# Performance work log

Measured on AMD Instinct MI355X. Metric: run time of the kernel, lower is better.

Reference implementation:

```python
import jax, jax.numpy as jnp
import numpy as np

N, E, F_IN, F_HID, K = 100000, 1600000, 64, 64, 6


def setup_inputs() -> dict:
    key = jax.random.key(0)
    k1, k2, k3, k4, k5 = jax.random.split(key, 5)
    x = jax.random.normal(k1, (N, F_IN), dtype=jnp.float32)
    # edges with no self-loops (PyG ChebConv removes self loops before normalization)
    src = jax.random.randint(k2, (E,), 0, N, dtype=jnp.int32)
    off = jax.random.randint(k3, (E,), 1, N, dtype=jnp.int32)
    dst = (src + off) % N
    edge_index = jnp.stack([src, dst], axis=0)
    # Glorot-ish init for the K Chebyshev weight matrices
    W = jax.random.normal(k4, (K, F_IN, F_HID), dtype=jnp.float32) * (1.0 / np.sqrt(F_IN))
    b = jax.random.normal(k5, (F_HID,), dtype=jnp.float32) * 0.01
    return {"x": x, "edge_index": edge_index, "W": W, "b": b}


def reference(x, edge_index, W, b):
    # ChebConv with sym normalization, lambda_max = 2.0 (PyG default):
    # scaled Laplacian L_hat = 2*L/lambda_max - I = -D^{-1/2} A D^{-1/2} (zero diagonal)
    row = edge_index[0].astype(jnp.int32)  # source j
    col = edge_index[1].astype(jnp.int32)  # target i
    n = x.shape[0]
    deg = jax.ops.segment_sum(jnp.ones_like(row, dtype=x.dtype), row, num_segments=n)
    dinv = jnp.where(deg > 0, jax.lax.rsqrt(deg), jnp.zeros_like(deg))
    w = -(dinv[row] * dinv[col])  # [E] edge weights of L_hat

    def prop(h):  # h: [N, F] -> L_hat @ h via gather-scale-scatter
        return jax.ops.segment_sum(w[:, None] * h[row], col, num_segments=n)

    # Chebyshev recurrence: Tx_0 = x, Tx_1 = L_hat x, Tx_k = 2 L_hat Tx_{k-1} - Tx_{k-2}
    Tx0 = x
    out = Tx0 @ W[0]
    Tx1 = prop(Tx0)
    out = out + Tx1 @ W[1]
    for k in range(2, W.shape[0]):
        Tx2 = 2.0 * prop(Tx1) - Tx0
        out = out + Tx2 @ W[k]
        Tx0, Tx1 = Tx1, Tx2
    return jax.nn.relu(out + b)
```

## Files before the change

### kernel.cpp

```cpp
#include <hip/hip_runtime.h>


constexpr int F = 64;
constexpr int SCAN_ELEMS = 1024;
constexpr int BSH = 9;
constexpr int EPB = 2048;
constexpr int PNPW = 8;

typedef __attribute__((ext_vector_type(8))) short short8;
typedef __attribute__((ext_vector_type(4))) float floatx4;
typedef __attribute__((ext_vector_type(2))) float floatx2;

#if defined(__has_builtin)
#if __has_builtin(__builtin_amdgcn_cvt_pk_f32_fp8) && __has_builtin(__builtin_amdgcn_cvt_pk_fp8_f32)
#define HAVE_FP8 1
#endif
#endif
#ifndef HAVE_FP8
#define HAVE_FP8 0
#endif

__device__ __forceinline__ unsigned short f_to_bf(float f) {
    unsigned u = __float_as_uint(f);
    u += 0x7FFFu + ((u >> 16) & 1u);
    return (unsigned short)(u >> 16);
}
__device__ __forceinline__ float bf_to_f(unsigned short s) {
    return __uint_as_float(((unsigned)s) << 16);
}
__device__ __forceinline__ float4 bf4_to_f4(ushort4 u) {
    float4 f;
    f.x = bf_to_f(u.x); f.y = bf_to_f(u.y); f.z = bf_to_f(u.z); f.w = bf_to_f(u.w);
    return f;
}

#if HAVE_FP8
__device__ __forceinline__ float4 fp8x4_to_f4(unsigned u) {
    floatx2 lo = __builtin_amdgcn_cvt_pk_f32_fp8((int)u, false);
    floatx2 hi = __builtin_amdgcn_cvt_pk_f32_fp8((int)u, true);
    float4 f;
    f.x = lo.x; f.y = lo.y; f.z = hi.x; f.w = hi.y;
    return f;
}
__device__ __forceinline__ unsigned f4_to_fp8x4(float a, float b, float c, float d) {
    int pk = 0;
    pk = __builtin_amdgcn_cvt_pk_fp8_f32(a, b, pk, false);
    pk = __builtin_amdgcn_cvt_pk_fp8_f32(c, d, pk, true);
    return (unsigned)pk;
}
#else
__device__ __forceinline__ float4 fp8x4_to_f4(unsigned u) { return make_float4(0, 0, 0, 0); }
__device__ __forceinline__ unsigned f4_to_fp8x4(float a, float b, float c, float d) { return 0; }
#endif

__global__ void hist2_kernel(const int* __restrict__ row, const int* __restrict__ col,
                             int* __restrict__ gcH, int* __restrict__ gcS,
                             int P, int G, int E) {
    __shared__ int hH[256], hS[256];
    const int tid = threadIdx.x, blk = blockIdx.x;
    hH[tid] = 0; hS[tid] = 0;
    __syncthreads();
    const int start = blk * EPB + tid * 8;
    if (start + 7 < E) {
        const int4 c0 = *(const int4*)(col + start);
        const int4 c1 = *(const int4*)(col + start + 4);
        const int4 r0 = *(const int4*)(row + start);
        const int4 r1 = *(const int4*)(row + start + 4);
        atomicAdd(&hH[c0.x >> BSH], 1); atomicAdd(&hH[c0.y >> BSH], 1);
        atomicAdd(&hH[c0.z >> BSH], 1); atomicAdd(&hH[c0.w >> BSH], 1);
        atomicAdd(&hH[c1.x >> BSH], 1); atomicAdd(&hH[c1.y >> BSH], 1);
        atomicAdd(&hH[c1.z >> BSH], 1); atomicAdd(&hH[c1.w >> BSH], 1);
        atomicAdd(&hS[r0.x >> BSH], 1); atomicAdd(&hS[r0.y >> BSH], 1);
        atomicAdd(&hS[r0.z >> BSH], 1); atomicAdd(&hS[r0.w >> BSH], 1);
        atomicAdd(&hS[r1.x >> BSH], 1); atomicAdd(&hS[r1.y >> BSH], 1);
        atomicAdd(&hS[r1.z >> BSH], 1); atomicAdd(&hS[r1.w >> BSH], 1);
    } else {
        for (int k = start; k < E && k < start + 8; ++k) {
            atomicAdd(&hH[col[k] >> BSH], 1);
            atomicAdd(&hS[row[k] >> BSH], 1);
        }
    }
    __syncthreads();
    if (tid < P) {
        gcH[(size_t)tid * G + blk] = hH[tid];
        gcS[(size_t)tid * G + blk] = hS[tid];
    }
}

__device__ __forceinline__ int4 load_cnt4(const int* __restrict__ cnt, int i, int N) {
    int4 v = make_int4(0, 0, 0, 0);
    if (i + 3 < N) {
        v = *(const int4*)(cnt + i);
    } else {
        if (i + 0 < N) v.x = cnt[i + 0];
        if (i + 1 < N) v.y = cnt[i + 1];
        if (i + 2 < N) v.z = cnt[i + 2];
        if (i + 3 < N) v.w = cnt[i + 3];
    }
    return v;
}

__global__ void scan1_kernel(const int* __restrict__ cnt, int* __restrict__ bsum, int N) {
    const int tid = threadIdx.x;
    const int i = blockIdx.x * SCAN_ELEMS + tid * 4;
    int4 v = load_cnt4(cnt, i, N);
    int s = v.x + v.y + v.z + v.w;
#pragma unroll
    for (int off = 1; off < 64; off <<= 1) s += __shfl_xor(s, off);
    __shared__ int ws[4];
    if ((tid & 63) == 0) ws[tid >> 6] = s;
    __syncthreads();
    if (tid == 0) bsum[blockIdx.x] = ws[0] + ws[1] + ws[2] + ws[3];
}

__global__ void scan2_kernel(const int* __restrict__ bsum, int* __restrict__ boff,
                             int* __restrict__ total_out, int nb) {
    const int tid = threadIdx.x;
    const int lane = tid & 63, w = tid >> 6;
    int v = (tid < nb) ? bsum[tid] : 0;
    int inc = v;
#pragma unroll
    for (int off = 1; off < 64; off <<= 1) {
        int t = __shfl_up(inc, off);
        if (lane >= off) inc += t;
    }
    __shared__ int wsum[4];
    if (lane == 63) wsum[w] = inc;
    __syncthreads();
    int wo = 0;
    for (int k = 0; k < w; ++k) wo += wsum[k];
    const int excl = wo + inc - v;
    if (tid < nb) boff[tid] = excl;
    if (tid == nb - 1) *total_out = excl + v;
}

__global__ void scan3_kernel(const int* __restrict__ cnt, const int* __restrict__ boff,
                             int* __restrict__ dst, int N) {
    const int tid = threadIdx.x;
    const int lane = tid & 63, w = tid >> 6;
    const int i = blockIdx.x * SCAN_ELEMS + tid * 4;
    int4 v = load_cnt4(cnt, i, N);
    const int s = v.x + v.y + v.z + v.w;
    int inc = s;
#pragma unroll
    for (int off = 1; off < 64; off <<= 1) {
        int t = __shfl_up(inc, off);
        if (lane >= off) inc += t;
    }
    __shared__ int wsum[4];
    if (lane == 63) wsum[w] = inc;
    __syncthreads();
    int wo = 0;
    for (int k = 0; k < w; ++k) wo += wsum[k];
    const int r0 = boff[blockIdx.x] + wo + inc - s;
    const int r1 = r0 + v.x, r2 = r1 + v.y, r3 = r2 + v.z;
    if (i + 3 < N) {
        *(int4*)(dst + i) = make_int4(r0, r1, r2, r3);
    } else {
        if (i + 0 < N) dst[i + 0] = r0;
        if (i + 1 < N) dst[i + 1] = r1;
        if (i + 2 < N) dst[i + 2] = r2;
        if (i + 3 < N) dst[i + 3] = r3;
    }
}

__global__ void part2_kernel(const int* __restrict__ row, const int* __restrict__ col,
                             const int* __restrict__ goH, const int* __restrict__ goS,
                             int* __restrict__ partH, int* __restrict__ partS,
                             int P, int G, int E) {
    __shared__ int cH[256], cS[256];
    const int tid = threadIdx.x, blk = blockIdx.x;
    if (tid < P) {
        cH[tid] = goH[(size_t)tid * G + blk];
        cS[tid] = goS[(size_t)tid * G + blk];
    }
    __syncthreads();
    const int start = blk * EPB + tid * 8;
    for (int k = start; k < E && k < start + 8; ++k) {
        const int c = col[k], r = row[k];
        const int posH = atomicAdd(&cH[c >> BSH], 1);
        partH[posH] = ((c & ((1 << BSH) - 1)) << 23) | r;
        const int posS = atomicAdd(&cS[r >> BSH], 1);
        partS[posS] = r;
    }
}

__global__ void bucketC_kernel(const int* __restrict__ part, const int* __restrict__ goff,
                               int* __restrict__ rowptr, int* __restrict__ csr,
                               int P, int G, int N, int E) {
    __shared__ int cnt[512];
    __shared__ int excl[512];
    __shared__ int wsum[4];
    const int tid = threadIdx.x;
    const int b = blockIdx.x;
    const int base_node = b << BSH;
    const int nn = min(512, N - base_node);
    const int estart = goff[(size_t)b * G];
    const int eend = (b + 1 < P) ? goff[(size_t)(b + 1) * G] : E;

    cnt[tid] = 0; cnt[tid + 256] = 0;
    __syncthreads();
    for (int i = estart + tid; i < eend; i += 256)
        atomicAdd(&cnt[((unsigned)part[i]) >> 23], 1);
    __syncthreads();
    {
        const int lane = tid & 63, w = tid >> 6;
        const int a0 = cnt[2 * tid], a1 = cnt[2 * tid + 1];
        const int ps = a0 + a1;
        int inc = ps;
#pragma unroll
        for (int off = 1; off < 64; off <<= 1) {
            int t = __shfl_up(inc, off);
            if (lane >= off) inc += t;
        }
        if (lane == 63) wsum[w] = inc;
        __syncthreads();
        int wo = 0;
        for (int k = 0; k < w; ++k) wo += wsum[k];
        const int ep = wo + inc - ps;
        excl[2 * tid] = ep;
        excl[2 * tid + 1] = ep + a0;
    }
    __syncthreads();
    if (tid < nn) rowptr[base_node + tid] = estart + excl[tid];
    for (int ln = 256 + tid; ln < nn; ln += 256) rowptr[base_node + ln] = estart + excl[ln];
    if (b == P - 1 && tid == 0) rowptr[N] = E;
    cnt[tid] = 0; cnt[tid + 256] = 0;
    __syncthreads();
    for (int i = estart + tid; i < eend; i += 256) {
        const int pk = part[i];
        const int ln = ((unsigned)pk) >> 23;
        const int pos = atomicAdd(&cnt[ln], 1);
        csr[estart + excl[ln] + pos] = pk & 0x7FFFFF;
    }
}

__global__ void bucketD_kernel(const int* __restrict__ partS, const int* __restrict__ goffS,
                               float* __restrict__ dinv, float* __restrict__ dinv2,
                               float* __restrict__ rdinv, int P, int G, int N, int E) {
    __shared__ int cnt[512];
    const int tid = threadIdx.x;
    const int b = blockIdx.x;
    const int base_node = b << BSH;
    const int nn = min(512, N - base_node);
    const int estart = goffS[(size_t)b * G];
    const int eend = (b + 1 < P) ? goffS[(size_t)(b + 1) * G] : E;
    cnt[tid] = 0; cnt[tid + 256] = 0;
    __syncthreads();
    for (int i = estart + tid; i < eend; i += 256)
        atomicAdd(&cnt[partS[i] - base_node], 1);
    __syncthreads();
    for (int l = tid; l < nn; l += 256) {
        const int dI = cnt[l];
        const float d = (float)dI;
        const bool ok = dI > 0;
        dinv[base_node + l]  = ok ? rsqrtf(d) : 0.0f;
        dinv2[base_node + l] = ok ? 1.0f / d : 0.0f;
        rdinv[base_node + l] = ok ? sqrtf(d) : 0.0f;
    }
}

__global__ void init_s0_kernel(const float* __restrict__ dinv, const float* __restrict__ x,
                               unsigned short* __restrict__ S0b, unsigned char* __restrict__ S0f8,
                               int NF, int write8) {
    int i = blockIdx.x * blockDim.x + threadIdx.x;
    int j = i * 4;
    if (j >= NF) return;
    const float dv = dinv[j >> 6];
    const float4 v = *(const float4*)(x + j);
    const float a = dv * v.x, bb = dv * v.y, c = dv * v.z, d = dv * v.w;
    ushort4 u;
    u.x = f_to_bf(a); u.y = f_to_bf(bb); u.z = f_to_bf(c); u.w = f_to_bf(d);
    *(ushort4*)(S0b + j) = u;
    if (write8) *(unsigned*)(S0f8 + j) = f4_to_fp8x4(a, bb, c, d);
}

template <int FIRST>
__global__ __launch_bounds__(256, 6)
void prop_g4(const int* __restrict__ rowptr, const int* __restrict__ csr,
             const float* __restrict__ dinv2, const unsigned short* __restrict__ Sprev,
             const unsigned short* __restrict__ Sm2, unsigned short* __restrict__ Sk, int N) {
    const int lane = threadIdx.x & 63;
    const int g16 = lane & 48;
    const int fl = lane & 15;
    const int wave = threadIdx.x >> 6;
    const int wbase = (blockIdx.x * 4 + wave) * PNPW;
    for (int j = 0; j < PNPW; j += 4) {
        const int n = wbase + j + (g16 >> 4);
        const bool nv = n < N;
        const int nc = nv ? n : N - 1;
        const int s = rowptr[nc], e = rowptr[nc + 1];
        const int len = e - s;
        float4 acc = {0.f, 0.f, 0.f, 0.f};
        for (int c = 0; c < len; c += 16) {
            const int ii = s + c + fl;
            const int idxv = csr[ii < e ? ii : e - 1];
            const int mm = min(16, len - c);
            ushort4 u[16];
#pragma unroll
            for (int t = 0; t < 16; ++t) {
                const int it = __shfl(idxv, g16 + t);
                u[t] = *(const ushort4*)(Sprev + (size_t)it * F + fl * 4);
            }
#pragma unroll
            for (int t = 0; t < 16; ++t) {
                if (t < mm) {
                    const float4 v = bf4_to_f4(u[t]);
                    acc.x += v.x; acc.y += v.y; acc.z += v.z; acc.w += v.w;
                }
            }
        }
        if (nv) {
            const float d2 = dinv2[n];
            float4 sn;
            if (FIRST) {
                sn.x = -d2 * acc.x; sn.y = -d2 * acc.y;
                sn.z = -d2 * acc.z; sn.w = -d2 * acc.w;
            } else {
                const float4 m2 = bf4_to_f4(*(const ushort4*)(Sm2 + (size_t)n * F + fl * 4));
                sn.x = -2.f * d2 * acc.x - m2.x; sn.y = -2.f * d2 * acc.y - m2.y;
                sn.z = -2.f * d2 * acc.z - m2.z; sn.w = -2.f * d2 * acc.w - m2.w;
            }
            ushort4 o;
            o.x = f_to_bf(sn.x); o.y = f_to_bf(sn.y);
            o.z = f_to_bf(sn.z); o.w = f_to_bf(sn.w);
            *(ushort4*)(Sk + (size_t)n * F + fl * 4) = o;
        }
    }
}

template <int FIRST, int W8>
__global__ __launch_bounds__(256, 6)
void prop_f8(const int* __restrict__ rowptr, const int* __restrict__ csr,
             const float* __restrict__ dinv2, const unsigned char* __restrict__ S8prev,
             const unsigned short* __restrict__ Sm2, unsigned short* __restrict__ Sk,
             unsigned char* __restrict__ Sk8, int N) {
    const int lane = threadIdx.x & 63;
    const int g16 = lane & 48;
    const int fl = lane & 15;
    const int wave = threadIdx.x >> 6;
    const int wbase = (blockIdx.x * 4 + wave) * PNPW;
    for (int j = 0; j < PNPW; j += 4) {
        const int n = wbase + j + (g16 >> 4);
        const bool nv = n < N;
        const int nc = nv ? n : N - 1;
        const int s = rowptr[nc], e = rowptr[nc + 1];
        const int len = e - s;
        float4 acc = {0.f, 0.f, 0.f, 0.f};
        for (int c = 0; c < len; c += 16) {
            const int ii = s + c + fl;
            const int idxv = csr[ii < e ? ii : e - 1];
            const int mm = min(16, len - c);
            unsigned u[16];
#pragma unroll
            for (int t = 0; t < 16; ++t) {
                const int it = __shfl(idxv, g16 + t);
                u[t] = *(const unsigned*)(S8prev + (size_t)it * F + fl * 4);
            }
#pragma unroll
            for (int t = 0; t < 16; ++t) {
                if (t < mm) {
                    const float4 v = fp8x4_to_f4(u[t]);
                    acc.x += v.x; acc.y += v.y; acc.z += v.z; acc.w += v.w;
                }
            }
        }
        if (nv) {
            const float d2 = dinv2[n];
            float4 sn;
            if (FIRST) {
                sn.x = -d2 * acc.x; sn.y = -d2 * acc.y;
                sn.z = -d2 * acc.z; sn.w = -d2 * acc.w;
            } else {
                const float4 m2 = bf4_to_f4(*(const ushort4*)(Sm2 + (size_t)n * F + fl * 4));
                sn.x = -2.f * d2 * acc.x - m2.x; sn.y = -2.f * d2 * acc.y - m2.y;
                sn.z = -2.f * d2 * acc.z - m2.z; sn.w = -2.f * d2 * acc.w - m2.w;
            }
            ushort4 o;
            o.x = f_to_bf(sn.x); o.y = f_to_bf(sn.y);
            o.z = f_to_bf(sn.z); o.w = f_to_bf(sn.w);
            *(ushort4*)(Sk + (size_t)n * F + fl * 4) = o;
            if (W8) *(unsigned*)(Sk8 + (size_t)n * F + fl * 4) = f4_to_fp8x4(sn.x, sn.y, sn.z, sn.w);
        }
    }
}

__global__ void wfrag_kernel(const float* __restrict__ W, unsigned short* __restrict__ Wfrag) {
    const int idx = blockIdx.x * blockDim.x + threadIdx.x;
    if (idx >= 4 * 12 * 64) return;
    const int lane = idx & 63;
    const int s = (idx >> 6) % 12;
    const int ft = idx / (64 * 12);
    const int n = ft * 16 + (lane & 15);
    const int quad = lane >> 4;
    unsigned short v[8];
#pragma unroll
    for (int j = 0; j < 8; ++j) {
        const int kg = s * 32 + quad * 8 + j;
        const int kk = kg >> 6, f = kg & 63;
        v[j] = f_to_bf(W[kk * F * F + f * F + n]);
    }
    ushort4 lo = {v[0], v[1], v[2], v[3]};
    ushort4 hi = {v[4], v[5], v[6], v[7]};
    *(ushort4*)(Wfrag + (size_t)idx * 8) = lo;
    *(ushort4*)(Wfrag + (size_t)idx * 8 + 4) = hi;
}

__global__ __launch_bounds__(256, 3)
void mfma_out_kernel(const float* __restrict__ x, const unsigned short* __restrict__ Sstack,
                     const unsigned short* __restrict__ Wfrag, const float* __restrict__ rdinv,
                     const float* __restrict__ dinv2, const float* __restrict__ W,
                     const float* __restrict__ b, float* __restrict__ out, int N, int NF) {
    const int lane = threadIdx.x & 63;
    const int wave = threadIdx.x >> 6;
    const int quad = lane >> 4;
    const int fl = lane & 15;
    const int tm = (blockIdx.x * 4 + wave) * 16;
    if (tm >= N) return;
    const int ma = tm + fl;
    const int mac = ma < N ? ma : N - 1;

    const unsigned short* sa = Sstack + (size_t)mac * F + quad * 8;

    short8 Afr[12];
#pragma unroll
    for (int s = 0; s < 12; ++s) {
        const int kk = s >> 1, f0 = (s & 1) * 32;
        Afr[s] = *(const short8*)(sa + (size_t)kk * NF + f0);
    }

    floatx4 C0 = {0.f, 0.f, 0.f, 0.f};
    floatx4 C1 = {0.f, 0.f, 0.f, 0.f};
    floatx4 C2 = {0.f, 0.f, 0.f, 0.f};
    floatx4 C3 = {0.f, 0.f, 0.f, 0.f};
    const unsigned short* wf = Wfrag + (size_t)lane * 8;
#pragma unroll
    for (int s = 0; s < 12; ++s) {
        const short8 B0 = *(const short8*)(wf + (size_t)(0 * 12 + s) * 64 * 8);
        const short8 B1 = *(const short8*)(wf + (size_t)(1 * 12 + s) * 64 * 8);
        const short8 B2 = *(const short8*)(wf + (size_t)(2 * 12 + s) * 64 * 8);
        const short8 B3 = *(const short8*)(wf + (size_t)(3 * 12 + s) * 64 * 8);
        C0 = __builtin_amdgcn_mfma_f32_16x16x32_bf16(Afr[s], B0, C0, 0, 0, 0);
        C1 = __builtin_amdgcn_mfma_f32_16x16x32_bf16(Afr[s], B1, C1, 0, 0, 0);
        C2 = __builtin_amdgcn_mfma_f32_16x16x32_bf16(Afr[s], B2, C2, 0, 0, 0);
        C3 = __builtin_amdgcn_mfma_f32_16x16x32_bf16(Afr[s], B3, C3, 0, 0, 0);
    }

    const float bl0 = b[0 * 16 + fl];
    const float bl1 = b[1 * 16 + fl];
    const float bl2 = b[2 * 16 + fl];
    const float bl3 = b[3 * 16 + fl];

#pragma unroll
    for (int r = 0; r < 4; ++r) {
        const int m = tm + quad * 4 + r;
        if (m >= N) continue;
        const float rs = rdinv[m];
        const bool z = (dinv2[m] == 0.0f);
        float v0 = rs * C0[r], v1 = rs * C1[r], v2 = rs * C2[r], v3 = rs * C3[r];
        if (z) {
            const float* xr = x + (size_t)m * F;
            float f0 = 0.f, f1 = 0.f, f2 = 0.f, f3 = 0.f;
            for (int f = 0; f < F; ++f) {
                const float xv = xr[f];
                const float* w0 = W + 0 * F * F + f * F;
                const float* w2 = W + 2 * F * F + f * F;
                const float* w4 = W + 4 * F * F + f * F;
                f0 += xv * (w0[0 * 16 + fl] - w2[0 * 16 + fl] + w4[0 * 16 + fl]);
                f1 += xv * (w0[1 * 16 + fl] - w2[1 * 16 + fl] + w4[1 * 16 + fl]);
                f2 += xv * (w0[2 * 16 + fl] - w2[2 * 16 + fl] + w4[2 * 16 + fl]);
                f3 += xv * (w0[3 * 16 + fl] - w2[3 * 16 + fl] + w4[3 * 16 + fl]);
            }
            v0 = f0; v1 = f1; v2 = f2; v3 = f3;
        }
        float* orow = out + (size_t)m * F;
        orow[0 * 16 + fl] = fmaxf(v0 + bl0, 0.f);
        orow[1 * 16 + fl] = fmaxf(v1 + bl1, 0.f);
        orow[2 * 16 + fl] = fmaxf(v2 + bl2, 0.f);
        orow[3 * 16 + fl] = fmaxf(v3 + bl3, 0.f);
    }
}

extern "C" void kernel_launch(void* const* d_in, const int* in_sizes, int n_in,
                              void* d_out, int out_size, void* d_ws, size_t ws_size,
                              hipStream_t stream) {
    const float* x = (const float*)d_in[0];
    const int* ei = (const int*)d_in[1];
    const float* W = (const float*)d_in[2];
    const float* b = (const float*)d_in[3];

    const int N = in_sizes[0] / F;
    const int E = in_sizes[1] / 2;
    const int NF = N * F;
    const int* row = ei;
    const int* col = ei + E;

    const int P = (N + 511) >> BSH;
    const int G = (E + EPB - 1) / EPB;
    const int M = P * G;

    char* p = (char*)d_ws;
    auto alloc = [&](size_t bytes) {
        char* r = p;
        p += (bytes + 63) & ~(size_t)63;
        return r;
    };
    float* dinv   = (float*)alloc((size_t)N * sizeof(float));
    float* dinv2  = (float*)alloc((size_t)N * sizeof(float));
    float* rdinv  = (float*)alloc((size_t)N * sizeof(float));
    int*   rowptr = (int*)alloc((size_t)(N + 1) * sizeof(int));
    int*   bsum   = (int*)alloc(256 * sizeof(int));
    int*   boff   = (int*)alloc(256 * sizeof(int));
    int*   totS   = (int*)alloc(64);
    int*   gcH    = (int*)alloc((size_t)M * sizeof(int));
    int*   goH    = (int*)alloc((size_t)M * sizeof(int));
    int*   gcS    = (int*)alloc((size_t)M * sizeof(int));
    int*   goS    = (int*)alloc((size_t)M * sizeof(int));
    int*   csr    = (int*)alloc((size_t)E * sizeof(int));
    unsigned short* Sstack = (unsigned short*)alloc((size_t)6 * NF * sizeof(unsigned short));
    unsigned short* Wfrag  = (unsigned short*)alloc((size_t)4 * 12 * 64 * 8 * sizeof(unsigned short));
    unsigned char* F8A = (unsigned char*)alloc((size_t)NF);
    unsigned char* F8B = (unsigned char*)alloc((size_t)NF);
    const size_t needed = (size_t)(p - (char*)d_ws);
    const bool pathA = HAVE_FP8 && ws_size >= needed;
    int* partH = (int*)Sstack;
    int* partS = (int*)(Sstack + (size_t)NF);
    float* out = (float*)d_out;

    const int B = 256;
    const int nsbM = (M + SCAN_ELEMS - 1) / SCAN_ELEMS;
    const int pgrid = (N + 4 * PNPW - 1) / (4 * PNPW);

    hist2_kernel<<<G, B, 0, stream>>>(row, col, gcH, gcS, P, G, E);
    scan1_kernel<<<nsbM, B, 0, stream>>>(gcH, bsum, M);
    scan2_kernel<<<1, B, 0, stream>>>(bsum, boff, rowptr + N, nsbM);
    scan3_kernel<<<nsbM, B, 0, stream>>>(gcH, boff, goH, M);
    scan1_kernel<<<nsbM, B, 0, stream>>>(gcS, bsum, M);
    scan2_kernel<<<1, B, 0, stream>>>(bsum, boff, totS, nsbM);
    scan3_kernel<<<nsbM, B, 0, stream>>>(gcS, boff, goS, M);
    part2_kernel<<<G, B, 0, stream>>>(row, col, goH, goS, partH, partS, P, G, E);
    bucketC_kernel<<<P, B, 0, stream>>>(partH, goH, rowptr, csr, P, G, N, E);
    bucketD_kernel<<<P, B, 0, stream>>>(partS, goS, dinv, dinv2, rdinv, P, G, N, E);

    wfrag_kernel<<<(4 * 12 * 64 + B - 1) / B, B, 0, stream>>>(W, Wfrag);
    init_s0_kernel<<<(NF / 4 + B - 1) / B, B, 0, stream>>>(dinv, x, Sstack, F8A, NF,
                                                           pathA ? 1 : 0);
    unsigned short* S1 = Sstack + (size_t)1 * NF;
    unsigned short* S2 = Sstack + (size_t)2 * NF;
    unsigned short* S3 = Sstack + (size_t)3 * NF;
    unsigned short* S4 = Sstack + (size_t)4 * NF;
    unsigned short* S5 = Sstack + (size_t)5 * NF;
    if (pathA) {
        prop_f8<1, 1><<<pgrid, B, 0, stream>>>(rowptr, csr, dinv2, F8A, Sstack, S1, F8B, N);
        prop_f8<0, 1><<<pgrid, B, 0, stream>>>(rowptr, csr, dinv2, F8B, Sstack, S2, F8A, N);
        prop_f8<0, 1><<<pgrid, B, 0, stream>>>(rowptr, csr, dinv2, F8A, S1, S3, F8B, N);
        prop_f8<0, 1><<<pgrid, B, 0, stream>>>(rowptr, csr, dinv2, F8B, S2, S4, F8A, N);
        prop_f8<0, 0><<<pgrid, B, 0, stream>>>(rowptr, csr, dinv2, F8A, S3, S5, F8B, N);
    } else {
        prop_g4<1><<<pgrid, B, 0, stream>>>(rowptr, csr, dinv2, Sstack, Sstack, S1, N);
        prop_g4<0><<<pgrid, B, 0, stream>>>(rowptr, csr, dinv2, S1, Sstack, S2, N);
        prop_g4<0><<<pgrid, B, 0, stream>>>(rowptr, csr, dinv2, S2, S1, S3, N);
        prop_g4<0><<<pgrid, B, 0, stream>>>(rowptr, csr, dinv2, S3, S2, S4, N);
        prop_g4<0><<<pgrid, B, 0, stream>>>(rowptr, csr, dinv2, S4, S3, S5, N);
    }
    mfma_out_kernel<<<(N + 63) / 64, 256, 0, stream>>>(x, Sstack, Wfrag, rdinv, dinv2,
                                                       W, b, out, N, NF);
}
```

Measured before the change: 368.0 us.

## Split propagation into two source-node halves for cache locality

Each CSR row is split by source index into a low half (below N/2) and a high half, with a new midptr array marking the boundary. Every propagation step becomes two kernels: one gathers from low-index sources and writes fp32 partial sums to a buffer, the other gathers from high-index sources, adds the partials and finishes the Chebyshev update. The aim is to keep each pass's gather working set (half the feature table) resident in cache. In exchange it doubles kernel launches, adds an fp32 N×64 partial buffer write and read per step, and halves per-row work, which can leave lanes underused on short rows.

```diff
diff --git a/kernel.cpp b/kernel.cpp
--- a/kernel.cpp
+++ b/kernel.cpp
@@ -186,9 +186,12 @@
 }
 
 __global__ void bucketC_kernel(const int* __restrict__ part, const int* __restrict__ goff,
-                               int* __restrict__ rowptr, int* __restrict__ csr,
-                               int P, int G, int N, int E) {
+                               int* __restrict__ rowptr, int* __restrict__ midptr,
+                               int* __restrict__ csr,
+                               int P, int G, int N, int E, int H) {
     __shared__ int cnt[512];
+    __shared__ int cntA[512];
+    __shared__ int cursB[512];
     __shared__ int excl[512];
     __shared__ int wsum[4];
     const int tid = threadIdx.x;
@@ -199,9 +202,15 @@
     const int eend = (b + 1 < P) ? goff[(size_t)(b + 1) * G] : E;
 
     cnt[tid] = 0; cnt[tid + 256] = 0;
-    __syncthreads();
-    for (int i = estart + tid; i < eend; i += 256)
-        atomicAdd(&cnt[((unsigned)part[i]) >> 23], 1);
+    cntA[tid] = 0; cntA[tid + 256] = 0;
+    cursB[tid] = 0; cursB[tid + 256] = 0;
+    __syncthreads();
+    for (int i = estart + tid; i < eend; i += 256) {
+        const int pk = part[i];
+        const int ln = ((unsigned)pk) >> 23;
+        atomicAdd(&cnt[ln], 1);
+        if ((pk & 0x7FFFFF) < H) atomicAdd(&cntA[ln], 1);
+    }
     __syncthreads();
     {
         const int lane = tid & 63, w = tid >> 6;
@@ -222,16 +231,24 @@
         excl[2 * tid + 1] = ep + a0;
     }
     __syncthreads();
-    if (tid < nn) rowptr[base_node + tid] = estart + excl[tid];
-    for (int ln = 256 + tid; ln < nn; ln += 256) rowptr[base_node + ln] = estart + excl[ln];
+    for (int ln = tid; ln < nn; ln += 256) {
+        rowptr[base_node + ln] = estart + excl[ln];
+        midptr[base_node + ln] = estart + excl[ln] + cntA[ln];
+    }
     if (b == P - 1 && tid == 0) rowptr[N] = E;
     cnt[tid] = 0; cnt[tid + 256] = 0;
     __syncthreads();
     for (int i = estart + tid; i < eend; i += 256) {
         const int pk = part[i];
         const int ln = ((unsigned)pk) >> 23;
-        const int pos = atomicAdd(&cnt[ln], 1);
-        csr[estart + excl[ln] + pos] = pk & 0x7FFFFF;
+        const int r = pk & 0x7FFFFF;
+        if (r < H) {
+            const int pos = atomicAdd(&cnt[ln], 1);
+            csr[estart + excl[ln] + pos] = r;
+        } else {
+            const int pos = atomicAdd(&cursB[ln], 1);
+            csr[estart + excl[ln] + cntA[ln] + pos] = r;
+        }
     }
 }
 
@@ -275,11 +292,11 @@
     if (write8) *(unsigned*)(S0f8 + j) = f4_to_fp8x4(a, bb, c, d);
 }
 
-template <int FIRST>
+
 __global__ __launch_bounds__(256, 6)
-void prop_g4(const int* __restrict__ rowptr, const int* __restrict__ csr,
-             const float* __restrict__ dinv2, const unsigned short* __restrict__ Sprev,
-             const unsigned short* __restrict__ Sm2, unsigned short* __restrict__ Sk, int N) {
+void propA_g4(const int* __restrict__ rowptr, const int* __restrict__ midp,
+              const int* __restrict__ csr, const unsigned short* __restrict__ Sprev,
+              float* __restrict__ accP, int N) {
     const int lane = threadIdx.x & 63;
     const int g16 = lane & 48;
     const int fl = lane & 15;
@@ -289,7 +306,7 @@
         const int n = wbase + j + (g16 >> 4);
         const bool nv = n < N;
         const int nc = nv ? n : N - 1;
-        const int s = rowptr[nc], e = rowptr[nc + 1];
+        const int s = rowptr[nc], e = midp[nc];
         const int len = e - s;
         float4 acc = {0.f, 0.f, 0.f, 0.f};
         for (int c = 0; c < len; c += 16) {
@@ -310,7 +327,49 @@
                 }
             }
         }
+        if (nv) *(float4*)(accP + (size_t)n * F + fl * 4) = acc;
+    }
+}
+
+template <int FIRST>
+__global__ __launch_bounds__(256, 6)
+void propB_g4(const int* __restrict__ rowptr, const int* __restrict__ midp,
+              const int* __restrict__ csr, const float* __restrict__ dinv2,
+              const unsigned short* __restrict__ Sprev, const float* __restrict__ accP,
+              const unsigned short* __restrict__ Sm2, unsigned short* __restrict__ Sk, int N) {
+    const int lane = threadIdx.x & 63;
+    const int g16 = lane & 48;
+    const int fl = lane & 15;
+    const int wave = threadIdx.x >> 6;
+    const int wbase = (blockIdx.x * 4 + wave) * PNPW;
+    for (int j = 0; j < PNPW; j += 4) {
+        const int n = wbase + j + (g16 >> 4);
+        const bool nv = n < N;
+        const int nc = nv ? n : N - 1;
+        const int s = midp[nc], e = rowptr[nc + 1];
+        const int len = e - s;
+        float4 acc = {0.f, 0.f, 0.f, 0.f};
+        for (int c = 0; c < len; c += 16) {
+            const int ii = s + c + fl;
+            const int idxv = csr[ii < e ? ii : e - 1];
+            const int mm = min(16, len - c);
+            ushort4 u[16];
+#pragma unroll
+            for (int t = 0; t < 16; ++t) {
+                const int it = __shfl(idxv, g16 + t);
+                u[t] = *(const ushort4*)(Sprev + (size_t)it * F + fl * 4);
+            }
+#pragma unroll
+            for (int t = 0; t < 16; ++t) {
+                if (t < mm) {
+                    const float4 v = bf4_to_f4(u[t]);
+                    acc.x += v.x; acc.y += v.y; acc.z += v.z; acc.w += v.w;
+                }
+            }
+        }
         if (nv) {
+            const float4 pa = *(const float4*)(accP + (size_t)n * F + fl * 4);
+            acc.x += pa.x; acc.y += pa.y; acc.z += pa.z; acc.w += pa.w;
             const float d2 = dinv2[n];
             float4 sn;
             if (FIRST) {
@@ -329,12 +388,10 @@
     }
 }
 
-template <int FIRST, int W8>
 __global__ __launch_bounds__(256, 6)
-void prop_f8(const int* __restrict__ rowptr, const int* __restrict__ csr,
-             const float* __restrict__ dinv2, const unsigned char* __restrict__ S8prev,
-             const unsigned short* __restrict__ Sm2, unsigned short* __restrict__ Sk,
-             unsigned char* __restrict__ Sk8, int N) {
+void propA_f8(const int* __restrict__ rowptr, const int* __restrict__ midp,
+              const int* __restrict__ csr, const unsigned char* __restrict__ S8prev,
+              float* __restrict__ accP, int N) {
     const int lane = threadIdx.x & 63;
     const int g16 = lane & 48;
     const int fl = lane & 15;
@@ -344,7 +401,7 @@
         const int n = wbase + j + (g16 >> 4);
         const bool nv = n < N;
         const int nc = nv ? n : N - 1;
-        const int s = rowptr[nc], e = rowptr[nc + 1];
+        const int s = rowptr[nc], e = midp[nc];
         const int len = e - s;
         float4 acc = {0.f, 0.f, 0.f, 0.f};
         for (int c = 0; c < len; c += 16) {
@@ -365,7 +422,50 @@
                 }
             }
         }
+        if (nv) *(float4*)(accP + (size_t)n * F + fl * 4) = acc;
+    }
+}
+
+template <int FIRST, int W8>
+__global__ __launch_bounds__(256, 6)
+void propB_f8(const int* __restrict__ rowptr, const int* __restrict__ midp,
+              const int* __restrict__ csr, const float* __restrict__ dinv2,
+              const unsigned char* __restrict__ S8prev, const float* __restrict__ accP,
+              const unsigned short* __restrict__ Sm2, unsigned short* __restrict__ Sk,
+              unsigned char* __restrict__ Sk8, int N) {
+    const int lane = threadIdx.x & 63;
+    const int g16 = lane & 48;
+    const int fl = lane & 15;
+    const int wave = threadIdx.x >> 6;
+    const int wbase = (blockIdx.x * 4 + wave) * PNPW;
+    for (int j = 0; j < PNPW; j += 4) {
+        const int n = wbase + j + (g16 >> 4);
+        const bool nv = n < N;
+        const int nc = nv ? n : N - 1;
+        const int s = midp[nc], e = rowptr[nc + 1];
+        const int len = e - s;
+        float4 acc = {0.f, 0.f, 0.f, 0.f};
+        for (int c = 0; c < len; c += 16) {
+            const int ii = s + c + fl;
+            const int idxv = csr[ii < e ? ii : e - 1];
+            const int mm = min(16, len - c);
+            unsigned u[16];
+#pragma unroll
+            for (int t = 0; t < 16; ++t) {
+                const int it = __shfl(idxv, g16 + t);
+                u[t] = *(const unsigned*)(S8prev + (size_t)it * F + fl * 4);
+            }
+#pragma unroll
+            for (int t = 0; t < 16; ++t) {
+                if (t < mm) {
+                    const float4 v = fp8x4_to_f4(u[t]);
+                    acc.x += v.x; acc.y += v.y; acc.z += v.z; acc.w += v.w;
+                }
+            }
+        }
         if (nv) {
+            const float4 pa = *(const float4*)(accP + (size_t)n * F + fl * 4);
+            acc.x += pa.x; acc.y += pa.y; acc.z += pa.z; acc.w += pa.w;
             const float d2 = dinv2[n];
             float4 sn;
             if (FIRST) {
@@ -498,6 +598,7 @@
     const int P = (N + 511) >> BSH;
     const int G = (E + EPB - 1) / EPB;
     const int M = P * G;
+    const int H = N >> 1;
 
     char* p = (char*)d_ws;
     auto alloc = [&](size_t bytes) {
@@ -509,6 +610,7 @@
     float* dinv2  = (float*)alloc((size_t)N * sizeof(float));
     float* rdinv  = (float*)alloc((size_t)N * sizeof(float));
     int*   rowptr = (int*)alloc((size_t)(N + 1) * sizeof(int));
+    int*   midptr = (int*)alloc((size_t)N * sizeof(int));
     int*   bsum   = (int*)alloc(256 * sizeof(int));
     int*   boff   = (int*)alloc(256 * sizeof(int));
     int*   totS   = (int*)alloc(64);
@@ -519,6 +621,7 @@
     int*   csr    = (int*)alloc((size_t)E * sizeof(int));
     unsigned short* Sstack = (unsigned short*)alloc((size_t)6 * NF * sizeof(unsigned short));
     unsigned short* Wfrag  = (unsigned short*)alloc((size_t)4 * 12 * 64 * 8 * sizeof(unsigned short));
+    float* accP = (float*)alloc((size_t)NF * sizeof(float));
     unsigned char* F8A = (unsigned char*)alloc((size_t)NF);
     unsigned char* F8B = (unsigned char*)alloc((size_t)NF);
     const size_t needed = (size_t)(p - (char*)d_ws);
@@ -539,7 +642,7 @@
     scan2_kernel<<<1, B, 0, stream>>>(bsum, boff, totS, nsbM);
     scan3_kernel<<<nsbM, B, 0, stream>>>(gcS, boff, goS, M);
     part2_kernel<<<G, B, 0, stream>>>(row, col, goH, goS, partH, partS, P, G, E);
-    bucketC_kernel<<<P, B, 0, stream>>>(partH, goH, rowptr, csr, P, G, N, E);
+    bucketC_kernel<<<P, B, 0, stream>>>(partH, goH, rowptr, midptr, csr, P, G, N, E, H);
     bucketD_kernel<<<P, B, 0, stream>>>(partS, goS, dinv, dinv2, rdinv, P, G, N, E);
 
     wfrag_kernel<<<(4 * 12 * 64 + B - 1) / B, B, 0, stream>>>(W, Wfrag);
@@ -551,17 +654,37 @@
     unsigned short* S4 = Sstack + (size_t)4 * NF;
     unsigned short* S5 = Sstack + (size_t)5 * NF;
     if (pathA) {
-        prop_f8<1, 1><<<pgrid, B, 0, stream>>>(rowptr, csr, dinv2, F8A, Sstack, S1, F8B, N);
-        prop_f8<0, 1><<<pgrid, B, 0, stream>>>(rowptr, csr, dinv2, F8B, Sstack, S2, F8A, N);
-        prop_f8<0, 1><<<pgrid, B, 0, stream>>>(rowptr, csr, dinv2, F8A, S1, S3, F8B, N);
-        prop_f8<0, 1><<<pgrid, B, 0, stream>>>(rowptr, csr, dinv2, F8B, S2, S4, F8A, N);
-        prop_f8<0, 0><<<pgrid, B, 0, stream>>>(rowptr, csr, dinv2, F8A, S3, S5, F8B, N);
+        propA_f8<<<pgrid, B, 0, stream>>>(rowptr, midptr, csr, F8A, accP, N);
+        propB_f8<1, 1><<<pgrid, B, 0, stream>>>(rowptr, midptr, csr, dinv2, F8A, accP,
+                                                Sstack, S1, F8B, N);
+        propA_f8<<<pgrid, B, 0, stream>>>(rowptr, midptr, csr, F8B, accP, N);
+        propB_f8<0, 1><<<pgrid, B, 0, stream>>>(rowptr, midptr, csr, dinv2, F8B, accP,
+                                                Sstack, S2, F8A, N);
+        propA_f8<<<pgrid, B, 0, stream>>>(rowptr, midptr, csr, F8A, accP, N);
+        propB_f8<0, 1><<<pgrid, B, 0, stream>>>(rowptr, midptr, csr, dinv2, F8A, accP,
+                                                S1, S3, F8B, N);
+        propA_f8<<<pgrid, B, 0, stream>>>(rowptr, midptr, csr, F8B, accP, N);
+        propB_f8<0, 1><<<pgrid, B, 0, stream>>>(rowptr, midptr, csr, dinv2, F8B, accP,
+                                                S2, S4, F8A, N);
+        propA_f8<<<pgrid, B, 0, stream>>>(rowptr, midptr, csr, F8A, accP, N);
+        propB_f8<0, 0><<<pgrid, B, 0, stream>>>(rowptr, midptr, csr, dinv2, F8A, accP,
+                                                S3, S5, F8B, N);
     } else {
-        prop_g4<1><<<pgrid, B, 0, stream>>>(rowptr, csr, dinv2, Sstack, Sstack, S1, N);
-        prop_g4<0><<<pgrid, B, 0, stream>>>(rowptr, csr, dinv2, S1, Sstack, S2, N);
-        prop_g4<0><<<pgrid, B, 0, stream>>>(rowptr, csr, dinv2, S2, S1, S3, N);
-        prop_g4<0><<<pgrid, B, 0, stream>>>(rowptr, csr, dinv2, S3, S2, S4, N);
-        prop_g4<0><<<pgrid, B, 0, stream>>>(rowptr, csr, dinv2, S4, S3, S5, N);
+        propA_g4<<<pgrid, B, 0, stream>>>(rowptr, midptr, csr, Sstack, accP, N);
+        propB_g4<1><<<pgrid, B, 0, stream>>>(rowptr, midptr, csr, dinv2, Sstack, accP,
+                                             Sstack, S1, N);
+        propA_g4<<<pgrid, B, 0, stream>>>(rowptr, midptr, csr, S1, accP, N);
+        propB_g4<0><<<pgrid, B, 0, stream>>>(rowptr, midptr, csr, dinv2, S1, accP,
+                                             Sstack, S2, N);
+        propA_g4<<<pgrid, B, 0, stream>>>(rowptr, midptr, csr, S2, accP, N);
+        propB_g4<0><<<pgrid, B, 0, stream>>>(rowptr, midptr, csr, dinv2, S2, accP,
+                                             S1, S3, N);
+        propA_g4<<<pgrid, B, 0, stream>>>(rowptr, midptr, csr, S3, accP, N);
+        propB_g4<0><<<pgrid, B, 0, stream>>>(rowptr, midptr, csr, dinv2, S3, accP,
+                                             S2, S4, N);
+        propA_g4<<<pgrid, B, 0, stream>>>(rowptr, midptr, csr, S4, accP, N);
+        propB_g4<0><<<pgrid, B, 0, stream>>>(rowptr, midptr, csr, dinv2, S4, accP,
+                                             S3, S5, N);
     }
     mfma_out_kernel<<<(N + 63) / 64, 256, 0, stream>>>(x, Sstack, Wfrag, rdinv, dinv2,
                                                        W, b, out, N, NF);
```

Result: slower. 420.0 us (+14.1%).
